# Kernel tuning notes

Measured on AMD Instinct MI355X. Metric: run time of the kernel, lower is better.

The kernel has to match this reference:

```python
import jax, jax.numpy as jnp
import numpy as np

ALPHA = 0.1
B, N, M = 384, 256, 64
EPS = 1e-5


def _lsa(cost):
    """Exact linear sum assignment (Jonker-Volgenant shortest augmenting path).
    cost: (n, m) with n <= m. Returns col4row: for each row, its assigned column.
    Matches scipy.optimize.linear_sum_assignment.
    """
    cost = np.asarray(cost, dtype=np.float64)
    n, m = cost.shape
    u = np.zeros(n)
    v = np.zeros(m)
    col4row = np.full(n, -1, dtype=np.int64)
    row4col = np.full(m, -1, dtype=np.int64)
    for cur_row in range(n):
        min_val = 0.0
        i = cur_row
        SR = np.zeros(n, dtype=bool)
        SC = np.zeros(m, dtype=bool)
        shortest = np.full(m, np.inf)
        prev = np.full(m, -1, dtype=np.int64)
        sink = -1
        while sink == -1:
            SR[i] = True
            rem = ~SC
            cols = np.nonzero(rem)[0]
            d = min_val + cost[i, cols] - u[i] - v[cols]
            upd = d < shortest[cols]
            shortest[cols[upd]] = d[upd]
            prev[cols[upd]] = i
            j = int(np.argmin(np.where(SC, np.inf, shortest)))
            min_val = shortest[j]
            SC[j] = True
            if row4col[j] == -1:
                sink = j
            else:
                i = row4col[j]
        # dual updates
        u[cur_row] += min_val
        sr = SR.copy()
        sr[cur_row] = False
        rows = np.nonzero(sr)[0]
        u[rows] += min_val - shortest[col4row[rows]]
        scc = np.nonzero(SC)[0]
        v[scc] -= min_val - shortest[scc]
        # augment along the alternating path
        j = sink
        while True:
            i = prev[j]
            row4col[j] = i
            col4row[i], j = j, col4row[i]
            if i == cur_row:
                break
    return col4row


def _assignments(pred_np, label_np, lens_np):
    """Build the (detached) one-hot assignment tensor X[b, pred, label]."""
    conf = pred_np[..., 3]
    log_c = np.log(conf + EPS)
    log_ca = np.log(1.0 - conf + EPS)
    X = np.zeros((pred_np.shape[0], pred_np.shape[1], label_np.shape[1]), dtype=np.float32)
    for b in range(pred_np.shape[0]):
        L = int(lens_np[b])
        diff = pred_np[b, :, None, :3] - label_np[b, None, :L, :]   # [N, L, 3]
        nd = (diff * diff).sum(-1)                                  # [N, L]
        C = ALPHA * nd / 2.0 - log_c[b][:, None] + log_ca[b][:, None]
        matched_preds = _lsa(C.T)                                   # [L] distinct pred indices
        X[b, matched_preds, np.arange(L)] = 1.0
    return X


def setup_inputs() -> dict:
    key = jax.random.key(0)
    k1, k2, k3 = jax.random.split(key, 3)
    pred = jax.random.uniform(k1, (B, N, 4), dtype=jnp.float32)      # coords + confidence in (0,1)
    label = jax.random.uniform(k2, (B, M, 3), dtype=jnp.float32)
    label_len = jax.random.randint(k3, (B,), 1, M + 1, dtype=jnp.int32)
    return {"pred": pred, "label": label, "label_len": label_len}


def reference(pred, label, label_len):
    # Host-side exact bipartite matching (detached, as in the torch original).
    X = jnp.asarray(_assignments(np.asarray(pred), np.asarray(label), np.asarray(label_len)))  # [B,N,M]
    x_c = 1.0 - X.sum(-1)                                   # [B,N] 1 for unmatched preds

    diff = pred[:, :, None, :3] - label[:, None, :, :]      # [B,N,M,3]
    normed = jnp.sum(diff * diff, axis=-1)                  # [B,N,M] squared L2
    conf = pred[:, :, 3]
    log_c = jnp.log(conf + EPS)
    log_ca = jnp.log(1.0 - conf + EPS)

    location_loss = jnp.sum(normed * X) / 2.0
    conf_pos_b = -jnp.einsum('bnm,bn->b', X, log_c)         # -(log_c_exp * X).sum per batch
    conf_neg_b = -jnp.sum(log_ca * x_c, axis=1)             # -(log_c_anti * x_c).sum per batch
    confidence_loss = jnp.sum(conf_pos_b + conf_neg_b + 1e-4)

    loss = ALPHA * location_loss + confidence_loss
    # Original returns last-batch confidence terms as diagnostics.
    return loss, ALPHA * location_loss, conf_pos_b[-1], conf_neg_b[-1]
```

## Files before the change

kernel.cpp:

```cpp
#include <hip/hip_runtime.h>
#include <math.h>


#define B_ 384
#define N_ 256
#define M_ 64

typedef unsigned long long u64;
typedef unsigned int u32;

#define WOFF   (1 << 20)
#define SCBIAS 0x30000000
#define DCLAMP 0x007FFFFE

static __device__ __forceinline__ float readlane_f32(float x, int l) {
  return __int_as_float(__builtin_amdgcn_readlane(__float_as_int(x), l));
}

static __device__ __forceinline__ int qcost(float px_, float py_, float pz_,
                                            float base_,
                                            float lx, float ly, float lz) {
  const float t1 = __fmul_rn(px_, lx);
  const float t2 = __fmaf_rn(py_, ly, t1);
  const float t3 = __fmaf_rn(pz_, lz, t2);
  return (int)__fmaf_rn(t3, -3276.8f, base_);
}

static __device__ __forceinline__ u32 wave_min_u32(u32 ck) {
  asm("s_nop 1\n\t"
      "v_min_u32_dpp %0, %0, %0 row_shr:1 row_mask:0xf bank_mask:0xf\n\t"
      "s_nop 1\n\t"
      "v_min_u32_dpp %0, %0, %0 row_shr:2 row_mask:0xf bank_mask:0xf\n\t"
      "s_nop 1\n\t"
      "v_min_u32_dpp %0, %0, %0 row_shr:4 row_mask:0xf bank_mask:0xf\n\t"
      "s_nop 1\n\t"
      "v_min_u32_dpp %0, %0, %0 row_shr:8 row_mask:0xf bank_mask:0xf\n\t"
      "s_nop 1\n\t"
      "v_min_u32_dpp %0, %0, %0 row_bcast:15 row_mask:0xa bank_mask:0xf\n\t"
      "s_nop 1\n\t"
      "v_min_u32_dpp %0, %0, %0 row_bcast:31 row_mask:0xc bank_mask:0xf"
      : "+v"(ck));
  return ck;
}

__global__ __launch_bounds__(64) void lsa_loss_kernel(
    const float* __restrict__ pred,
    const float* __restrict__ label,
    const int* __restrict__ label_len,
    double* __restrict__ ws,
    float* __restrict__ out)
{
  const int b = blockIdx.x;
  const int lane = threadIdx.x;

  __shared__ float lab_x[M_], lab_y[M_], lab_z[M_];

  const float* lp = label + (size_t)(b * M_ + lane) * 3;
  const float labx = lp[0], laby = lp[1], labz = lp[2];
  lab_x[lane] = labx; lab_y[lane] = laby; lab_z[lane] = labz;

  float px[4], py[4], pz[4], lc[4], lca[4], base[4];
  int v[4];
  int scb[4];
  const float4* pred4 = reinterpret_cast<const float4*>(pred);
#pragma unroll
  for (int k = 0; k < 4; ++k) {
    const float4 p = pred4[b * N_ + lane + 64 * k];
    px[k] = p.x; py[k] = p.y; pz[k] = p.z;
    lc[k]  = logf(__fadd_rn(p.w, 1e-5f));
    lca[k] = logf(__fadd_rn(__fsub_rn(1.0f, p.w), 1e-5f));
    const float qgf = __fmul_rn(__fsub_rn(lca[k], lc[k]), 32768.0f);
    const float npp = __fmaf_rn(p.z, p.z, __fmaf_rn(p.y, p.y, __fmul_rn(p.x, p.x)));
    base[k] = __fmaf_rn(npp, 1638.4f, qgf);
    v[k] = 0;
    scb[k] = 0;
  }
  int rfc[4] = {-1, -1, -1, -1};
  int c4r = -1;
  int u_reg = 0;

  int L = label_len[b];
  L = (L < 1) ? 1 : ((L > M_) ? M_ : L);

  __syncthreads();

  for (int r = 0; r < L; ++r) {
    const float lx = readlane_f32(labx, r);
    const float ly = readlane_f32(laby, r);
    const float lz = readlane_f32(labz, r);
    u32 cand[4];
#pragma unroll
    for (int k = 0; k < 4; ++k) {
      const int j = lane + 64 * k;
      const int q = qcost(px[k], py[k], pz[k], base[k], lx, ly, lz);
      cand[k] = ((u32)(q + WOFF) << 8) | (u32)j;
    }
    const u32 m01 = (cand[0] < cand[1]) ? cand[0] : cand[1];
    const u32 m23 = (cand[2] < cand[3]) ? cand[2] : cand[3];
    u32 ck = wave_min_u32((m01 < m23) ? m01 : m23);
    const u32 wk = (u32)__builtin_amdgcn_readlane((int)ck, 63);
    const int j1 = (int)(wk & 0xFF);
    if (lane == r) u_reg = (int)(wk >> 8) - WOFF;
    const int kk1 = j1 >> 6;
    const int lsel = j1 & 63;
    const int t0 = __builtin_amdgcn_readlane(rfc[0], lsel);
    const int t1 = __builtin_amdgcn_readlane(rfc[1], lsel);
    const int t2 = __builtin_amdgcn_readlane(rfc[2], lsel);
    const int t3 = __builtin_amdgcn_readlane(rfc[3], lsel);
    const int taken = (kk1 == 0) ? t0 : (kk1 == 1) ? t1 : (kk1 == 2) ? t2 : t3;
    if (taken < 0) {
      const bool selfc = (lane == lsel);
      rfc[0] = (selfc && kk1 == 0) ? r : rfc[0];
      rfc[1] = (selfc && kk1 == 1) ? r : rfc[1];
      rfc[2] = (selfc && kk1 == 2) ? r : rfc[2];
      rfc[3] = (selfc && kk1 == 3) ? r : rfc[3];
      if (lane == r) c4r = j1;
    }
  }
  u64 free_mask = __ballot((lane < L) && (c4r < 0));

  while (free_mask) {
    const int cur_row = (int)__builtin_ctzll(free_mask);
    free_mask &= free_mask - 1;

    u32 shk[4] = {0x7FFFFFFFu, 0x7FFFFFFFu, 0x7FFFFFFFu, 0x7FFFFFFFu};
    int pv[4] = {0, 0, 0, 0};
    int mv_join = 0;
    int joined = 0;
    int min_val = 0;
    int i_cur = cur_row;
    int u_i = __builtin_amdgcn_readlane(u_reg, i_cur);
    float lx = readlane_f32(labx, i_cur);
    float ly = readlane_f32(laby, i_cur);
    float lz = readlane_f32(labz, i_cur);
    int t = 0 - u_i;
    int sink = -1;

    while (true) {
      int tv[4];
#pragma unroll
      for (int k = 0; k < 4; ++k) tv[k] = (t - v[k]) + scb[k];

      u32 cand[4];
#pragma unroll
      for (int k = 0; k < 4; ++k) {
        const int j = lane + 64 * k;
        int dd = qcost(px[k], py[k], pz[k], base[k], lx, ly, lz) + tv[k];
        dd = (dd < DCLAMP) ? dd : DCLAMP;
        const u32 key = ((u32)dd << 8) | (u32)j;
        const bool upd = key < shk[k];
        shk[k] = upd ? key : shk[k];
        pv[k]  = upd ? i_cur : pv[k];
        cand[k] = key;
      }
      const u32 m01 = (cand[0] < cand[1]) ? cand[0] : cand[1];
      const u32 m23 = (cand[2] < cand[3]) ? cand[2] : cand[3];
      u32 ck = wave_min_u32((m01 < m23) ? m01 : m23);
      const u32 wk = (u32)__builtin_amdgcn_readlane((int)ck, 63);
      const int j_min = (int)(wk & 0xFF);
      min_val = (int)(wk >> 8);
      const int kk = j_min >> 6;
      const int lsel = j_min & 63;
      const bool selfc = (lane == lsel);
      scb[0] += (selfc && kk == 0) ? SCBIAS : 0;
      scb[1] += (selfc && kk == 1) ? SCBIAS : 0;
      scb[2] += (selfc && kk == 2) ? SCBIAS : 0;
      scb[3] += (selfc && kk == 3) ? SCBIAS : 0;
      const int r0 = __builtin_amdgcn_readlane(rfc[0], lsel);
      const int r1 = __builtin_amdgcn_readlane(rfc[1], lsel);
      const int r2 = __builtin_amdgcn_readlane(rfc[2], lsel);
      const int r3 = __builtin_amdgcn_readlane(rfc[3], lsel);
      const int r4 = (kk == 0) ? r0 : (kk == 1) ? r1 : (kk == 2) ? r2 : r3;
      if (r4 < 0) { sink = j_min; break; }
      i_cur = r4;
      if (lane == i_cur) { mv_join = min_val; joined = 1; }
      u_i = __builtin_amdgcn_readlane(u_reg, i_cur);
      lx = readlane_f32(labx, i_cur);
      ly = readlane_f32(laby, i_cur);
      lz = readlane_f32(labz, i_cur);
      t = min_val - u_i;
    }

    if (lane == cur_row)  u_reg += min_val;
    else if (joined)      u_reg += min_val - mv_join;
#pragma unroll
    for (int k = 0; k < 4; ++k) {
      if (scb[k]) {
        v[k] -= (min_val - (int)(shk[k] >> 8));
        scb[k] = 0;
      }
    }

    {
      int j = sink;
      while (true) {
        const int kkj = j >> 6, lj = j & 63;
        const int p0 = __builtin_amdgcn_readlane(pv[0], lj);
        const int p1 = __builtin_amdgcn_readlane(pv[1], lj);
        const int p2 = __builtin_amdgcn_readlane(pv[2], lj);
        const int p3 = __builtin_amdgcn_readlane(pv[3], lj);
        const int ii = (kkj == 0) ? p0 : (kkj == 1) ? p1 : (kkj == 2) ? p2 : p3;
        const bool self = (lane == lj);
        rfc[0] = (self && kkj == 0) ? ii : rfc[0];
        rfc[1] = (self && kkj == 1) ? ii : rfc[1];
        rfc[2] = (self && kkj == 2) ? ii : rfc[2];
        rfc[3] = (self && kkj == 3) ? ii : rfc[3];
        const int jn = __builtin_amdgcn_readlane(c4r, ii);
        if (lane == ii) c4r = j;
        if (ii == cur_row) break;
        j = jn;
      }
    }
  }

  double loc = 0.0, cpos = 0.0, cneg = 0.0;
#pragma unroll
  for (int k = 0; k < 4; ++k) {
    const int l = rfc[k];
    if (l >= 0) {
      const float d0 = __fsub_rn(px[k], lab_x[l]);
      const float d1 = __fsub_rn(py[k], lab_y[l]);
      const float d2 = __fsub_rn(pz[k], lab_z[l]);
      const float nd = __fadd_rn(__fadd_rn(__fmul_rn(d0, d0), __fmul_rn(d1, d1)),
                                 __fmul_rn(d2, d2));
      loc += (double)nd;
      cpos -= (double)lc[k];
    } else {
      cneg -= (double)lca[k];
    }
  }
  for (int off = 32; off >= 1; off >>= 1) {
    loc += __shfl_xor(loc, off, 64);
    cpos += __shfl_xor(cpos, off, 64);
    cneg += __shfl_xor(cneg, off, 64);
  }

  if (lane == 0) {
    atomicAdd(&ws[0], loc);
    atomicAdd(&ws[1], cpos + cneg + 1e-4);
    if (b == B_ - 1) { atomicAdd(&ws[2], cpos); atomicAdd(&ws[3], cneg); }
    __threadfence();
    unsigned int* cnt = (unsigned int*)(ws + 4);
    const unsigned int old = atomicAdd(cnt, 1u);
    if (old == (unsigned int)(B_ - 1)) {
      __threadfence();
      const double loc_t  = atomicAdd(&ws[0], 0.0);
      const double conf_t = atomicAdd(&ws[1], 0.0);
      const double cpos_l = atomicAdd(&ws[2], 0.0);
      const double cneg_l = atomicAdd(&ws[3], 0.0);
      const double lloc = 0.1 * (loc_t * 0.5);
      out[0] = (float)(lloc + conf_t);
      out[1] = (float)lloc;
      out[2] = (float)cpos_l;
      out[3] = (float)cneg_l;
    }
  }
}

extern "C" void kernel_launch(void* const* d_in, const int* in_sizes, int n_in,
                              void* d_out, int out_size, void* d_ws, size_t ws_size,
                              hipStream_t stream) {
  const float* pred = (const float*)d_in[0];
  const float* label = (const float*)d_in[1];
  const int* label_len = (const int*)d_in[2];
  double* ws = (double*)d_ws;
  float* out = (float*)d_out;

  hipMemsetAsync(d_ws, 0, 64, stream);
  lsa_loss_kernel<<<B_, 64, 0, stream>>>(pred, label, label_len, ws, out);
}
```

Baseline: 171.7 us.

## Drop per-column row arrays; derive ownership via ballot and pack prev into shortest keys

```diff
diff --git a/kernel.cpp b/kernel.cpp
--- a/kernel.cpp
+++ b/kernel.cpp
@@ -10,8 +10,9 @@
 typedef unsigned int u32;
 
 #define WOFF   (1 << 20)
-#define SCBIAS 0x30000000
 #define DCLAMP 0x007FFFFE
+#define BIGF   3.0e8f
+#define THF    1.0e8f
 
 static __device__ __forceinline__ float readlane_f32(float x, int l) {
   return __int_as_float(__builtin_amdgcn_readlane(__float_as_int(x), l));
@@ -26,21 +27,21 @@
   return (int)__fmaf_rn(t3, -3276.8f, base_);
 }
 
-static __device__ __forceinline__ u32 wave_min_u32(u32 ck) {
+static __device__ __forceinline__ void wave_min2_u32(u32& a, u32& b) {
   asm("s_nop 1\n\t"
       "v_min_u32_dpp %0, %0, %0 row_shr:1 row_mask:0xf bank_mask:0xf\n\t"
-      "s_nop 1\n\t"
+      "v_min_u32_dpp %1, %1, %1 row_shr:1 row_mask:0xf bank_mask:0xf\n\t"
       "v_min_u32_dpp %0, %0, %0 row_shr:2 row_mask:0xf bank_mask:0xf\n\t"
-      "s_nop 1\n\t"
+      "v_min_u32_dpp %1, %1, %1 row_shr:2 row_mask:0xf bank_mask:0xf\n\t"
       "v_min_u32_dpp %0, %0, %0 row_shr:4 row_mask:0xf bank_mask:0xf\n\t"
-      "s_nop 1\n\t"
+      "v_min_u32_dpp %1, %1, %1 row_shr:4 row_mask:0xf bank_mask:0xf\n\t"
       "v_min_u32_dpp %0, %0, %0 row_shr:8 row_mask:0xf bank_mask:0xf\n\t"
-      "s_nop 1\n\t"
+      "v_min_u32_dpp %1, %1, %1 row_shr:8 row_mask:0xf bank_mask:0xf\n\t"
       "v_min_u32_dpp %0, %0, %0 row_bcast:15 row_mask:0xa bank_mask:0xf\n\t"
-      "s_nop 1\n\t"
-      "v_min_u32_dpp %0, %0, %0 row_bcast:31 row_mask:0xc bank_mask:0xf"
-      : "+v"(ck));
-  return ck;
+      "v_min_u32_dpp %1, %1, %1 row_bcast:15 row_mask:0xa bank_mask:0xf\n\t"
+      "v_min_u32_dpp %0, %0, %0 row_bcast:31 row_mask:0xc bank_mask:0xf\n\t"
+      "v_min_u32_dpp %1, %1, %1 row_bcast:31 row_mask:0xc bank_mask:0xf"
+      : "+v"(a), "+v"(b));
 }
 
 __global__ __launch_bounds__(64) void lsa_loss_kernel(
@@ -54,14 +55,15 @@
   const int lane = threadIdx.x;
 
   __shared__ float lab_x[M_], lab_y[M_], lab_z[M_];
+  __shared__ int r4c_lds[N_];
 
   const float* lp = label + (size_t)(b * M_ + lane) * 3;
   const float labx = lp[0], laby = lp[1], labz = lp[2];
   lab_x[lane] = labx; lab_y[lane] = laby; lab_z[lane] = labz;
 
-  float px[4], py[4], pz[4], lc[4], lca[4], base[4];
+  float px[4], py[4], pz[4], lc[4], lca[4], base[4], baseO[4], baseB[4];
   int v[4];
-  int scb[4];
+  u32 jc[4];
   const float4* pred4 = reinterpret_cast<const float4*>(pred);
 #pragma unroll
   for (int k = 0; k < 4; ++k) {
@@ -71,11 +73,12 @@
     lca[k] = logf(__fadd_rn(__fsub_rn(1.0f, p.w), 1e-5f));
     const float qgf = __fmul_rn(__fsub_rn(lca[k], lc[k]), 32768.0f);
     const float npp = __fmaf_rn(p.z, p.z, __fmaf_rn(p.y, p.y, __fmul_rn(p.x, p.x)));
-    base[k] = __fmaf_rn(npp, 1638.4f, qgf);
+    base[k]  = __fmaf_rn(npp, 1638.4f, qgf);
+    baseO[k] = base[k];
+    baseB[k] = base[k] + BIGF;
     v[k] = 0;
-    scb[k] = 0;
-  }
-  int rfc[4] = {-1, -1, -1, -1};
+    jc[k] = (u32)(lane + 64 * k);
+  }
   int c4r = -1;
   int u_reg = 0;
 
@@ -91,31 +94,19 @@
     u32 cand[4];
 #pragma unroll
     for (int k = 0; k < 4; ++k) {
-      const int j = lane + 64 * k;
       const int q = qcost(px[k], py[k], pz[k], base[k], lx, ly, lz);
-      cand[k] = ((u32)(q + WOFF) << 8) | (u32)j;
-    }
-    const u32 m01 = (cand[0] < cand[1]) ? cand[0] : cand[1];
-    const u32 m23 = (cand[2] < cand[3]) ? cand[2] : cand[3];
-    u32 ck = wave_min_u32((m01 < m23) ? m01 : m23);
-    const u32 wk = (u32)__builtin_amdgcn_readlane((int)ck, 63);
+      cand[k] = ((u32)(q + WOFF) << 8) | jc[k];
+    }
+    u32 ca = (cand[0] < cand[1]) ? cand[0] : cand[1];
+    u32 cb = (cand[2] < cand[3]) ? cand[2] : cand[3];
+    wave_min2_u32(ca, cb);
+    const u32 wa = (u32)__builtin_amdgcn_readlane((int)ca, 63);
+    const u32 wb = (u32)__builtin_amdgcn_readlane((int)cb, 63);
+    const u32 wk = (wa < wb) ? wa : wb;
     const int j1 = (int)(wk & 0xFF);
     if (lane == r) u_reg = (int)(wk >> 8) - WOFF;
-    const int kk1 = j1 >> 6;
-    const int lsel = j1 & 63;
-    const int t0 = __builtin_amdgcn_readlane(rfc[0], lsel);
-    const int t1 = __builtin_amdgcn_readlane(rfc[1], lsel);
-    const int t2 = __builtin_amdgcn_readlane(rfc[2], lsel);
-    const int t3 = __builtin_amdgcn_readlane(rfc[3], lsel);
-    const int taken = (kk1 == 0) ? t0 : (kk1 == 1) ? t1 : (kk1 == 2) ? t2 : t3;
-    if (taken < 0) {
-      const bool selfc = (lane == lsel);
-      rfc[0] = (selfc && kk1 == 0) ? r : rfc[0];
-      rfc[1] = (selfc && kk1 == 1) ? r : rfc[1];
-      rfc[2] = (selfc && kk1 == 2) ? r : rfc[2];
-      rfc[3] = (selfc && kk1 == 3) ? r : rfc[3];
-      if (lane == r) c4r = j1;
-    }
+    const bool taken = __ballot(c4r == j1) != 0ull;
+    if (!taken && lane == r) c4r = j1;
   }
   u64 free_mask = __ballot((lane < L) && (c4r < 0));
 
@@ -124,10 +115,7 @@
     free_mask &= free_mask - 1;
 
     u32 shk[4] = {0x7FFFFFFFu, 0x7FFFFFFFu, 0x7FFFFFFFu, 0x7FFFFFFFu};
-    int pv[4] = {0, 0, 0, 0};
-    int mv_join = 0;
-    int joined = 0;
-    int min_val = 0;
+    int mvj = 0, joined = 0, min_val = 0;
     int i_cur = cur_row;
     int u_i = __builtin_amdgcn_readlane(u_reg, i_cur);
     float lx = readlane_f32(labx, i_cur);
@@ -137,43 +125,36 @@
     int sink = -1;
 
     while (true) {
-      int tv[4];
-#pragma unroll
-      for (int k = 0; k < 4; ++k) tv[k] = (t - v[k]) + scb[k];
-
       u32 cand[4];
 #pragma unroll
       for (int k = 0; k < 4; ++k) {
-        const int j = lane + 64 * k;
-        int dd = qcost(px[k], py[k], pz[k], base[k], lx, ly, lz) + tv[k];
+        const int tv = t - v[k];
+        int dd = qcost(px[k], py[k], pz[k], base[k], lx, ly, lz) + tv;
         dd = (dd < DCLAMP) ? dd : DCLAMP;
-        const u32 key = ((u32)dd << 8) | (u32)j;
-        const bool upd = key < shk[k];
-        shk[k] = upd ? key : shk[k];
-        pv[k]  = upd ? i_cur : pv[k];
-        cand[k] = key;
+        const u32 rkey = ((u32)dd << 8) | jc[k];
+        const u32 skey = ((u32)dd << 8) | (u32)i_cur;
+        shk[k] = (skey < shk[k]) ? skey : shk[k];
+        cand[k] = rkey;
       }
-      const u32 m01 = (cand[0] < cand[1]) ? cand[0] : cand[1];
-      const u32 m23 = (cand[2] < cand[3]) ? cand[2] : cand[3];
-      u32 ck = wave_min_u32((m01 < m23) ? m01 : m23);
-      const u32 wk = (u32)__builtin_amdgcn_readlane((int)ck, 63);
+      u32 ca = (cand[0] < cand[1]) ? cand[0] : cand[1];
+      u32 cb = (cand[2] < cand[3]) ? cand[2] : cand[3];
+      wave_min2_u32(ca, cb);
+      const u32 wa = (u32)__builtin_amdgcn_readlane((int)ca, 63);
+      const u32 wb = (u32)__builtin_amdgcn_readlane((int)cb, 63);
+      const u32 wk = (wa < wb) ? wa : wb;
       const int j_min = (int)(wk & 0xFF);
       min_val = (int)(wk >> 8);
       const int kk = j_min >> 6;
-      const int lsel = j_min & 63;
-      const bool selfc = (lane == lsel);
-      scb[0] += (selfc && kk == 0) ? SCBIAS : 0;
-      scb[1] += (selfc && kk == 1) ? SCBIAS : 0;
-      scb[2] += (selfc && kk == 2) ? SCBIAS : 0;
-      scb[3] += (selfc && kk == 3) ? SCBIAS : 0;
-      const int r0 = __builtin_amdgcn_readlane(rfc[0], lsel);
-      const int r1 = __builtin_amdgcn_readlane(rfc[1], lsel);
-      const int r2 = __builtin_amdgcn_readlane(rfc[2], lsel);
-      const int r3 = __builtin_amdgcn_readlane(rfc[3], lsel);
-      const int r4 = (kk == 0) ? r0 : (kk == 1) ? r1 : (kk == 2) ? r2 : r3;
-      if (r4 < 0) { sink = j_min; break; }
-      i_cur = r4;
-      if (lane == i_cur) { mv_join = min_val; joined = 1; }
+      const bool selfc = (lane == (j_min & 63));
+      base[0] = (selfc && kk == 0) ? baseB[0] : base[0];
+      base[1] = (selfc && kk == 1) ? baseB[1] : base[1];
+      base[2] = (selfc && kk == 2) ? baseB[2] : base[2];
+      base[3] = (selfc && kk == 3) ? baseB[3] : base[3];
+      const bool own = (c4r == j_min);
+      const u64 om = __ballot(own);
+      if (om == 0ull) { sink = j_min; break; }
+      i_cur = (int)__builtin_ctzll(om);
+      if (own) { mvj = min_val; joined = 1; }
       u_i = __builtin_amdgcn_readlane(u_reg, i_cur);
       lx = readlane_f32(labx, i_cur);
       ly = readlane_f32(laby, i_cur);
@@ -182,12 +163,12 @@
     }
 
     if (lane == cur_row)  u_reg += min_val;
-    else if (joined)      u_reg += min_val - mv_join;
+    else if (joined)      u_reg += min_val - mvj;
 #pragma unroll
     for (int k = 0; k < 4; ++k) {
-      if (scb[k]) {
+      if (base[k] > THF) {
         v[k] -= (min_val - (int)(shk[k] >> 8));
-        scb[k] = 0;
+        base[k] = baseO[k];
       }
     }
 
@@ -195,16 +176,12 @@
       int j = sink;
       while (true) {
         const int kkj = j >> 6, lj = j & 63;
-        const int p0 = __builtin_amdgcn_readlane(pv[0], lj);
-        const int p1 = __builtin_amdgcn_readlane(pv[1], lj);
-        const int p2 = __builtin_amdgcn_readlane(pv[2], lj);
-        const int p3 = __builtin_amdgcn_readlane(pv[3], lj);
-        const int ii = (kkj == 0) ? p0 : (kkj == 1) ? p1 : (kkj == 2) ? p2 : p3;
-        const bool self = (lane == lj);
-        rfc[0] = (self && kkj == 0) ? ii : rfc[0];
-        rfc[1] = (self && kkj == 1) ? ii : rfc[1];
-        rfc[2] = (self && kkj == 2) ? ii : rfc[2];
-        rfc[3] = (self && kkj == 3) ? ii : rfc[3];
+        const int s0 = __builtin_amdgcn_readlane((int)shk[0], lj);
+        const int s1 = __builtin_amdgcn_readlane((int)shk[1], lj);
+        const int s2 = __builtin_amdgcn_readlane((int)shk[2], lj);
+        const int s3 = __builtin_amdgcn_readlane((int)shk[3], lj);
+        const int ps = (kkj == 0) ? s0 : (kkj == 1) ? s1 : (kkj == 2) ? s2 : s3;
+        const int ii = ps & 0xFF;
         const int jn = __builtin_amdgcn_readlane(c4r, ii);
         if (lane == ii) c4r = j;
         if (ii == cur_row) break;
@@ -213,10 +190,16 @@
     }
   }
 
+#pragma unroll
+  for (int k = 0; k < 4; ++k) r4c_lds[lane + 64 * k] = -1;
+  __syncthreads();
+  if (c4r >= 0) r4c_lds[c4r] = lane;
+  __syncthreads();
+
   double loc = 0.0, cpos = 0.0, cneg = 0.0;
 #pragma unroll
   for (int k = 0; k < 4; ++k) {
-    const int l = rfc[k];
+    const int l = r4c_lds[lane + 64 * k];
     if (l >= 0) {
       const float d0 = __fsub_rn(px[k], lab_x[l]);
       const float d1 = __fsub_rn(py[k], lab_y[l]);
```

Measured after the change: 153.2 us (median of 2 runs). 10.7% less time.
